# Kernel optimization log

Hardware: AMD Instinct MI355X
Metric: run time of the kernel (lower is better)

The kernel has to match this reference:

```python
import jax, jax.numpy as jnp
import numpy as np

N = 10000      # nodes
E = 160000     # edges
D_IN = 512
D_H = 512
P_DROP = 0.2


def _glorot(key, shape):
    lim = float(np.sqrt(6.0 / (shape[0] + shape[1])))
    return jax.random.uniform(key, shape, jnp.float32, -lim, lim)


def setup_inputs() -> dict:
    key = jax.random.key(0)
    ks = jax.random.split(key, 8)
    h = jax.random.normal(ks[0], (N, D_IN), jnp.float32)
    src = jax.random.randint(ks[1], (E,), 0, N)
    dst = jax.random.randint(ks[2], (E,), 0, N)
    edge_weight = jax.random.uniform(ks[3], (E,), jnp.float32)
    W0 = _glorot(ks[4], (D_IN, D_H))
    W1 = _glorot(ks[5], (D_H, D_H))
    W2 = _glorot(ks[6], (D_H, D_H))
    b0 = jnp.zeros((D_H,), jnp.float32)
    b1 = jnp.zeros((D_H,), jnp.float32)
    b2 = jnp.zeros((D_H,), jnp.float32)
    return dict(h=h, src=src, dst=dst, edge_weight=edge_weight,
                W0=W0, b0=b0, W1=W1, b1=b1, W2=W2, b2=b2)


def _dropout(x, key):
    keep = jax.random.bernoulli(key, 1.0 - P_DROP, x.shape)
    return jnp.where(keep, x / (1.0 - P_DROP), 0.0)


def _graph_conv(x, src, dst, ew, W, b, act):
    # DGL GraphConv, norm='both', weight=True, bias=True, with edge_weight.
    ones = jnp.ones((src.shape[0],), x.dtype)
    deg_out = jnp.maximum(jax.ops.segment_sum(ones, src, num_segments=N), 1.0)
    deg_in = jnp.maximum(jax.ops.segment_sum(ones, dst, num_segments=N), 1.0)
    x = x * (deg_out ** -0.5)[:, None]          # src norm
    msg = x[src] * ew[:, None]                  # [E, D] gather + edge weight
    agg = jax.ops.segment_sum(msg, dst, num_segments=N)  # scatter-add
    out = (agg @ W) * (deg_in ** -0.5)[:, None] + b
    return act(out) if act is not None else out


def reference(h, src, dst, edge_weight, W0, b0, W1, b1, W2, b2):
    dk = jax.random.split(jax.random.key(42), 3)
    x = _dropout(h, dk[0])
    x = _graph_conv(x, src, dst, edge_weight, W0, b0, jax.nn.elu)
    x = _dropout(x, dk[1])
    x = _graph_conv(x, src, dst, edge_weight, W1, b1, jax.nn.elu)
    x = _dropout(x, dk[2])
    x = _graph_conv(x, src, dst, edge_weight, W2, b2, None)
    return x
```

## Files before the change

kernel.cpp:

```cpp
#include <hip/hip_runtime.h>
#include <stdint.h>

#define N_NODES 10000
#define N_EDGES 160000
#define D 512
#define TOT (N_NODES * D)
#define M_PAD 10112
#define NMASK (TOT / 32)
#define AGG_BLKS 2500
#define MASK_BLKS 625

typedef _Float16 h8 __attribute__((ext_vector_type(8)));
typedef float f4 __attribute__((ext_vector_type(4)));

__host__ __device__ inline uint32_t rotl32(uint32_t v, int r) {
    return (v << r) | (v >> (32 - r));
}

__host__ __device__ inline void tf2x32(uint32_t k0, uint32_t k1,
                                       uint32_t& x0, uint32_t& x1) {
    uint32_t k2 = k0 ^ k1 ^ 0x1BD11BDAu;
    x0 += k0; x1 += k1;
    x0 += x1; x1 = rotl32(x1, 13); x1 ^= x0;
    x0 += x1; x1 = rotl32(x1, 15); x1 ^= x0;
    x0 += x1; x1 = rotl32(x1, 26); x1 ^= x0;
    x0 += x1; x1 = rotl32(x1,  6); x1 ^= x0;
    x0 += k1; x1 += k2 + 1u;
    x0 += x1; x1 = rotl32(x1, 17); x1 ^= x0;
    x0 += x1; x1 = rotl32(x1, 29); x1 ^= x0;
    x0 += x1; x1 = rotl32(x1, 16); x1 ^= x0;
    x0 += x1; x1 = rotl32(x1, 24); x1 ^= x0;
    x0 += k2; x1 += k0 + 2u;
    x0 += x1; x1 = rotl32(x1, 13); x1 ^= x0;
    x0 += x1; x1 = rotl32(x1, 15); x1 ^= x0;
    x0 += x1; x1 = rotl32(x1, 26); x1 ^= x0;
    x0 += x1; x1 = rotl32(x1,  6); x1 ^= x0;
    x0 += k0; x1 += k1 + 3u;
    x0 += x1; x1 = rotl32(x1, 17); x1 ^= x0;
    x0 += x1; x1 = rotl32(x1, 29); x1 ^= x0;
    x0 += x1; x1 = rotl32(x1, 16); x1 ^= x0;
    x0 += x1; x1 = rotl32(x1, 24); x1 ^= x0;
    x0 += k1; x1 += k2 + 4u;
    x0 += x1; x1 = rotl32(x1, 13); x1 ^= x0;
    x0 += x1; x1 = rotl32(x1, 15); x1 ^= x0;
    x0 += x1; x1 = rotl32(x1, 26); x1 ^= x0;
    x0 += x1; x1 = rotl32(x1,  6); x1 ^= x0;
    x0 += k2; x1 += k0 + 5u;
}

__device__ __forceinline__ uint32_t dropout_bit(uint32_t k0, uint32_t k1, uint32_t j) {
    uint32_t c0 = 0u, c1 = j;
    tf2x32(k0, k1, c0, c1);
    uint32_t bits = c0 ^ c1;
    float u = __uint_as_float((bits >> 9) | 0x3f800000u) - 1.0f;
    return (u < 0.8f) ? 1u : 0u;
}

#define HIST_BLKS 625
#define WCONV_BLKS 192
#define PRE_BLKS (HIST_BLKS + WCONV_BLKS + 5000)
__global__ __launch_bounds__(256)
void pre_kernel(const int* __restrict__ src, const int* __restrict__ dst,
                int* __restrict__ deg_out, int* __restrict__ deg_in,
                const float* __restrict__ W0, const float* __restrict__ W1,
                const float* __restrict__ W2, _Float16* __restrict__ Wt,
                const float* __restrict__ x, _Float16* __restrict__ y,
                uint32_t k0, uint32_t k1) {
    __shared__ float tile[64][65];
    int b = blockIdx.x;
    int t = threadIdx.x;
    if (b < HIST_BLKS) {
        int e = b * 256 + t;
        if (e < N_EDGES) {
            atomicAdd(&deg_out[src[e]], 1);
            atomicAdd(&deg_in[dst[e]], 1);
        }
    } else if (b < HIST_BLKS + WCONV_BLKS) {
        int b2 = b - HIST_BLKS;
        int bx = b2 & 7, by = (b2 >> 3) & 7, bz = b2 >> 6;
        const float* W = (bz == 0) ? W0 : (bz == 1) ? W1 : W2;
        _Float16* T = Wt + (size_t)bz * 512 * 512;
        int r0 = by * 64, c0 = bx * 64;
        int c = t & 63, rq = t >> 6;
#pragma unroll
        for (int i = 0; i < 16; ++i) {
            int r = rq + i * 4;
            tile[r][c] = W[(size_t)(r0 + r) * 512 + c0 + c];
        }
        __syncthreads();
        int k = t & 63, nq = t >> 6;
#pragma unroll
        for (int i = 0; i < 16; ++i) {
            int n = nq + i * 4;
            T[(size_t)(c0 + n) * 512 + r0 + k] = (_Float16)tile[k][n];
        }
    } else {
        int b3 = b - HIST_BLKS - WCONV_BLKS;
        int j = (b3 * 256 + t) * 4;
        if (j >= TOT) return;
        float4 xv = *(const float4*)&x[j];
        _Float16 r[4];
        uint32_t jj = (uint32_t)j;
#pragma unroll
        for (int i = 0; i < 4; ++i) {
            float g = dropout_bit(k0, k1, jj + (uint32_t)i) ? 1.0f : 0.0f;
            float xi = (&xv.x)[i];
            r[i] = (_Float16)(g * (xi * 1.25f));
        }
        *(ushort4*)&y[j] = *(ushort4*)r;
    }
}

__global__ __launch_bounds__(1024)
void scan_kernel(const int* __restrict__ deg_in, const int* __restrict__ deg_out,
                 int* __restrict__ row_ptr,
                 float* __restrict__ rn_in, float* __restrict__ rn_out) {
    __shared__ int wsum[16];
    int tid = threadIdx.x;
    int lane = tid & 63, wv = tid >> 6;
    int base = tid * 10;
    int v[10];
    int tot = 0;
#pragma unroll
    for (int i = 0; i < 10; ++i) {
        int idx = base + i;
        v[i] = (idx < N_NODES) ? deg_in[idx] : 0;
        tot += v[i];
    }
    int s = tot;
#pragma unroll
    for (int off = 1; off < 64; off <<= 1) {
        int t = __shfl_up(s, off, 64);
        if (lane >= off) s += t;
    }
    if (lane == 63) wsum[wv] = s;
    __syncthreads();
    if (wv == 0 && lane < 16) {
        int ws = wsum[lane];
#pragma unroll
        for (int off = 1; off < 16; off <<= 1) {
            int t = __shfl_up(ws, off, 64);
            if (lane >= off) ws += t;
        }
        wsum[lane] = ws;
    }
    __syncthreads();
    int run = ((wv > 0) ? wsum[wv - 1] : 0) + (s - tot);
#pragma unroll
    for (int i = 0; i < 10; ++i) {
        int idx = base + i;
        if (idx < N_NODES) {
            row_ptr[idx] = run;
            rn_in[idx]  = 1.0f / sqrtf(fmaxf((float)v[i], 1.0f));
            rn_out[idx] = 1.0f / sqrtf(fmaxf((float)deg_out[idx], 1.0f));
        }
        run += v[i];
    }
    if (tid == 1023) row_ptr[N_NODES] = wsum[15];
}

__global__ void fill_kernel(const int* __restrict__ src, const int* __restrict__ dst,
                            const float* __restrict__ ew, const int* __restrict__ row_ptr,
                            const float* __restrict__ rn_out,
                            int* __restrict__ cursor, int2* __restrict__ csr) {
    int e = blockIdx.x * 256 + threadIdx.x;
    if (e >= N_EDGES) return;
    int v = dst[e];
    int sn = src[e];
    int pos = atomicAdd(&cursor[v], 1);
    int idx = row_ptr[v] + pos;
    csr[idx] = make_int2(sn, __float_as_int(ew[e] * rn_out[sn]));
}

__global__ __launch_bounds__(256)
void aggregate_kernel(const _Float16* __restrict__ y, const int* __restrict__ row_ptr,
                      const int2* __restrict__ csr, _Float16* __restrict__ agg,
                      uint32_t* __restrict__ mask, uint32_t mk0, uint32_t mk1) {
    int b = blockIdx.x;
    if (b >= AGG_BLKS) {
        if (mask == nullptr) return;
        int gtid = (b - AGG_BLKS) * 256 + threadIdx.x;
        if (gtid < NMASK) {
            uint32_t w = 0, jb = (uint32_t)gtid * 32u;
#pragma unroll 4
            for (int i = 0; i < 32; ++i)
                w |= dropout_bit(mk0, mk1, jb + (uint32_t)i) << i;
            mask[gtid] = w;
        }
        return;
    }
    int node = b * 4 + (threadIdx.x >> 6);
    int lane = threadIdx.x & 63;
    int beg = row_ptr[node], end = row_ptr[node + 1];
    const _Float16* yl = y + lane * 8;
    float acc[8] = {0, 0, 0, 0, 0, 0, 0, 0};
    int k = beg;
    for (; k + 7 < end; k += 8) {
        int2 e[8];
#pragma unroll
        for (int i = 0; i < 8; ++i) e[i] = csr[k + i];
        h8 v[8];
#pragma unroll
        for (int i = 0; i < 8; ++i) v[i] = *(const h8*)&yl[(size_t)e[i].x * 512];
#pragma unroll
        for (int i = 0; i < 8; ++i) {
            float w = __int_as_float(e[i].y);
#pragma unroll
            for (int j = 0; j < 8; ++j) acc[j] += w * (float)v[i][j];
        }
    }
    for (; k < end; ++k) {
        int2 e0 = csr[k];
        float w = __int_as_float(e0.y);
        h8 v = *(const h8*)&yl[(size_t)e0.x * 512];
#pragma unroll
        for (int j = 0; j < 8; ++j) acc[j] += w * (float)v[j];
    }
    _Float16 r[8];
#pragma unroll
    for (int j = 0; j < 8; ++j) r[j] = (_Float16)acc[j];
    *(h8*)&agg[(size_t)node * 512 + lane * 8] = *(h8*)r;
}

#define GBK 128
#define LDA2 136
__global__ __launch_bounds__(256)
void gemm_kernel(const _Float16* __restrict__ A, const _Float16* __restrict__ Wt,
                 const float* __restrict__ bias, const float* __restrict__ rn_in,
                 _Float16* __restrict__ yout, float* __restrict__ fout,
                 int mode, const uint32_t* __restrict__ mask) {
    __shared__ _Float16 As[64 * LDA2];
    __shared__ _Float16 Bs[64 * LDA2];
    int tid = threadIdx.x;
    int wv = tid >> 6, lane = tid & 63;

    int f = blockIdx.x;
    int T = (f & 7) * 158 + (f >> 3);
    int row0 = (T >> 3) * 64, col0 = (T & 7) * 64;

    int wr = wv >> 1, wc = wv & 1;

    f4 acc[2][2];
#pragma unroll
    for (int i = 0; i < 2; ++i)
#pragma unroll
        for (int j = 0; j < 2; ++j) acc[i][j] = (f4){0.f, 0.f, 0.f, 0.f};

    int r = tid >> 2;
    int cseg = (tid & 3) * 32;
    const _Float16* gA = A  + (size_t)(row0 + r) * 512 + cseg;
    const _Float16* gB = Wt + (size_t)(col0 + r) * 512 + cseg;
    _Float16* wA = &As[r * LDA2 + cseg];
    _Float16* wB = &Bs[r * LDA2 + cseg];

    const _Float16* fa = &As[(wr * 32 + (lane & 15)) * LDA2 + (lane >> 4) * 8];
    const _Float16* fb = &Bs[(wc * 32 + (lane & 15)) * LDA2 + (lane >> 4) * 8];

    h8 ra[4], rb[4];
#pragma unroll
    for (int i = 0; i < 4; ++i) {
        ra[i] = *(const h8*)(gA + i * 8);
        rb[i] = *(const h8*)(gB + i * 8);
    }

    for (int kk = 0; kk < 512; kk += GBK) {
#pragma unroll
        for (int i = 0; i < 4; ++i) {
            *(h8*)(wA + i * 8) = ra[i];
            *(h8*)(wB + i * 8) = rb[i];
        }
        __syncthreads();
        if (kk + GBK < 512) {
#pragma unroll
            for (int i = 0; i < 4; ++i) {
                ra[i] = *(const h8*)(gA + kk + GBK + i * 8);
                rb[i] = *(const h8*)(gB + kk + GBK + i * 8);
            }
        }
#pragma unroll
        for (int s = 0; s < 4; ++s) {
            h8 af0 = *(const h8*)(fa + s * 32);
            h8 af1 = *(const h8*)(fa + 16 * LDA2 + s * 32);
            h8 bf0 = *(const h8*)(fb + s * 32);
            h8 bf1 = *(const h8*)(fb + 16 * LDA2 + s * 32);
            acc[0][0] = __builtin_amdgcn_mfma_f32_16x16x32_f16(af0, bf0, acc[0][0], 0, 0, 0);
            acc[0][1] = __builtin_amdgcn_mfma_f32_16x16x32_f16(af0, bf1, acc[0][1], 0, 0, 0);
            acc[1][0] = __builtin_amdgcn_mfma_f32_16x16x32_f16(af1, bf0, acc[1][0], 0, 0, 0);
            acc[1][1] = __builtin_amdgcn_mfma_f32_16x16x32_f16(af1, bf1, acc[1][1], 0, 0, 0);
        }
        __syncthreads();
    }

    int mbase = row0 + wr * 32;
    int nbase = col0 + wc * 32;
#pragma unroll
    for (int mt = 0; mt < 2; ++mt) {
#pragma unroll
        for (int nt = 0; nt < 2; ++nt) {
            int gr0 = mbase + mt * 16 + (lane >> 4) * 4;
            int gc = nbase + nt * 16 + (lane & 15);
            float bcol = bias[gc];
#pragma unroll
            for (int i = 0; i < 4; ++i) {
                int gr = gr0 + i;
                if (gr >= N_NODES) continue;
                float v = acc[mt][nt][i] * rn_in[gr] + bcol;
                if (mode == 0) {
                    v = (v > 0.f) ? v : (__expf(v) - 1.0f);
                    uint32_t j = (uint32_t)(gr * 512 + gc);
                    uint32_t g = (mask[j >> 5] >> (j & 31)) & 1u;
                    v = g ? (v * 1.25f) : 0.0f;
                    yout[(size_t)gr * 512 + gc] = (_Float16)v;
                } else {
                    fout[(size_t)gr * 512 + gc] = v;
                }
            }
        }
    }
}

extern "C" void kernel_launch(void* const* d_in, const int* in_sizes, int n_in,
                              void* d_out, int out_size, void* d_ws, size_t ws_size,
                              hipStream_t stream) {
    const float* h   = (const float*)d_in[0];
    const int*   src = (const int*)d_in[1];
    const int*   dst = (const int*)d_in[2];
    const float* ew  = (const float*)d_in[3];
    const float* W0  = (const float*)d_in[4];
    const float* b0  = (const float*)d_in[5];
    const float* W1  = (const float*)d_in[6];
    const float* b1  = (const float*)d_in[7];
    const float* W2  = (const float*)d_in[8];
    const float* b2  = (const float*)d_in[9];
    const float* bl[3] = {b0, b1, b2};
    float* out = (float*)d_out;

    char* ws = (char*)d_ws;
    _Float16* y16  = (_Float16*)ws; ws += (size_t)TOT * 2;
    _Float16* aggF = (_Float16*)ws; ws += (size_t)M_PAD * 512 * 2;
    _Float16* Wt   = (_Float16*)ws; ws += (size_t)3 * 512 * 512 * 2;
    int* degi_in  = (int*)ws;  ws += N_NODES * 4;
    int* degi_out = (int*)ws;  ws += N_NODES * 4;
    int* cursor   = (int*)ws;  ws += N_NODES * 4;
    int* row_ptr  = (int*)ws;  ws += (N_NODES + 1) * 4;
    ws = (char*)(((uintptr_t)ws + 15) & ~(uintptr_t)15);
    int2* csr     = (int2*)ws; ws += (size_t)N_EDGES * 8;
    float* rn_in  = (float*)ws; ws += N_NODES * 4;
    float* rn_out = (float*)ws; ws += N_NODES * 4;
    uint32_t* maskbuf = (uint32_t*)ws; ws += (size_t)NMASK * 4;

    hipMemsetAsync(degi_in, 0, 3 * N_NODES * 4, stream);

    uint32_t dk[3][2];
    for (int i = 0; i < 3; ++i) {
        uint32_t c0 = 0u, c1 = (uint32_t)i;
        tf2x32(0u, 42u, c0, c1);
        dk[i][0] = c0; dk[i][1] = c1;
    }

    pre_kernel<<<PRE_BLKS, 256, 0, stream>>>(src, dst, degi_out, degi_in,
                                             W0, W1, W2, Wt, h, y16,
                                             dk[0][0], dk[0][1]);
    scan_kernel<<<1, 1024, 0, stream>>>(degi_in, degi_out, row_ptr, rn_in, rn_out);
    fill_kernel<<<(N_EDGES + 255) / 256, 256, 0, stream>>>(src, dst, ew, row_ptr,
                                                           rn_out, cursor, csr);

    for (int l = 0; l < 3; ++l) {
        uint32_t* mk = (l < 2) ? maskbuf : nullptr;
        uint32_t mk0 = (l < 2) ? dk[l + 1][0] : 0u;
        uint32_t mk1 = (l < 2) ? dk[l + 1][1] : 0u;
        aggregate_kernel<<<AGG_BLKS + MASK_BLKS, 256, 0, stream>>>(
            y16, row_ptr, csr, aggF, mk, mk0, mk1);
        int mode = (l < 2) ? 0 : 1;
        gemm_kernel<<<1264, 256, 0, stream>>>(
            aggF, Wt + (size_t)l * 512 * 512, bl[l], rn_in,
            y16, out, mode, maskbuf);
    }
}
```

Before: 316.3 us.

## Fuse neighbor aggregation and GEMM per 16-node tile with ping-pong buffers

Replaces the separate aggregate and GEMM kernels with one fused kernel per layer. Each 64-thread block gathers 16 nodes' neighbor features into LDS, then multiplies them by the full 512x512 weight using MFMA, applying the bias/ELU/dropout epilogue in place. Both dropout masks are now generated up front in the pre-kernel into separate buffers, and activations ping-pong between two buffers. This removes the intermediate aggregate round trip through memory and two launches per layer. In exchange, only 625 single-wave blocks run, giving low occupancy to hide gather latency, and every block re-reads the whole weight matrix from cache.

```diff
diff --git a/kernel.cpp b/kernel.cpp
--- a/kernel.cpp
+++ b/kernel.cpp
@@ -5,10 +5,7 @@
 #define N_EDGES 160000
 #define D 512
 #define TOT (N_NODES * D)
-#define M_PAD 10112
 #define NMASK (TOT / 32)
-#define AGG_BLKS 2500
-#define MASK_BLKS 625
 
 typedef _Float16 h8 __attribute__((ext_vector_type(8)));
 typedef float f4 __attribute__((ext_vector_type(4)));
@@ -58,14 +55,18 @@
 
 #define HIST_BLKS 625
 #define WCONV_BLKS 192
-#define PRE_BLKS (HIST_BLKS + WCONV_BLKS + 5000)
+#define DROP_BLKS 5000
+#define MASKG_BLKS 625
+#define PRE_BLKS (HIST_BLKS + WCONV_BLKS + DROP_BLKS + 2 * MASKG_BLKS)
 __global__ __launch_bounds__(256)
 void pre_kernel(const int* __restrict__ src, const int* __restrict__ dst,
                 int* __restrict__ deg_out, int* __restrict__ deg_in,
                 const float* __restrict__ W0, const float* __restrict__ W1,
                 const float* __restrict__ W2, _Float16* __restrict__ Wt,
                 const float* __restrict__ x, _Float16* __restrict__ y,
-                uint32_t k0, uint32_t k1) {
+                uint32_t k0, uint32_t k1,
+                uint32_t m1k0, uint32_t m1k1, uint32_t* __restrict__ mask1,
+                uint32_t m2k0, uint32_t m2k1, uint32_t* __restrict__ mask2) {
     __shared__ float tile[64][65];
     int b = blockIdx.x;
     int t = threadIdx.x;
@@ -94,7 +95,7 @@
             int n = nq + i * 4;
             T[(size_t)(c0 + n) * 512 + r0 + k] = (_Float16)tile[k][n];
         }
-    } else {
+    } else if (b < HIST_BLKS + WCONV_BLKS + DROP_BLKS) {
         int b3 = b - HIST_BLKS - WCONV_BLKS;
         int j = (b3 * 256 + t) * 4;
         if (j >= TOT) return;
@@ -108,6 +109,18 @@
             r[i] = (_Float16)(g * (xi * 1.25f));
         }
         *(ushort4*)&y[j] = *(ushort4*)r;
+    } else {
+        int b4 = b - HIST_BLKS - WCONV_BLKS - DROP_BLKS;
+        int which = b4 / MASKG_BLKS;
+        int gtid = (b4 % MASKG_BLKS) * 256 + t;
+        uint32_t mk0 = which ? m2k0 : m1k0;
+        uint32_t mk1 = which ? m2k1 : m1k1;
+        uint32_t* m = which ? mask2 : mask1;
+        uint32_t w = 0, jb = (uint32_t)gtid * 32u;
+#pragma unroll 4
+        for (int i = 0; i < 32; ++i)
+            w |= dropout_bit(mk0, mk1, jb + (uint32_t)i) << i;
+        m[gtid] = w;
     }
 }
 
@@ -172,150 +185,125 @@
     csr[idx] = make_int2(sn, __float_as_int(ew[e] * rn_out[sn]));
 }
 
-__global__ __launch_bounds__(256)
-void aggregate_kernel(const _Float16* __restrict__ y, const int* __restrict__ row_ptr,
-                      const int2* __restrict__ csr, _Float16* __restrict__ agg,
-                      uint32_t* __restrict__ mask, uint32_t mk0, uint32_t mk1) {
-    int b = blockIdx.x;
-    if (b >= AGG_BLKS) {
-        if (mask == nullptr) return;
-        int gtid = (b - AGG_BLKS) * 256 + threadIdx.x;
-        if (gtid < NMASK) {
-            uint32_t w = 0, jb = (uint32_t)gtid * 32u;
-#pragma unroll 4
-            for (int i = 0; i < 32; ++i)
-                w |= dropout_bit(mk0, mk1, jb + (uint32_t)i) << i;
-            mask[gtid] = w;
-        }
-        return;
-    }
-    int node = b * 4 + (threadIdx.x >> 6);
-    int lane = threadIdx.x & 63;
-    int beg = row_ptr[node], end = row_ptr[node + 1];
-    const _Float16* yl = y + lane * 8;
-    float acc[8] = {0, 0, 0, 0, 0, 0, 0, 0};
-    int k = beg;
-    for (; k + 7 < end; k += 8) {
-        int2 e[8];
-#pragma unroll
-        for (int i = 0; i < 8; ++i) e[i] = csr[k + i];
-        h8 v[8];
-#pragma unroll
-        for (int i = 0; i < 8; ++i) v[i] = *(const h8*)&yl[(size_t)e[i].x * 512];
-#pragma unroll
-        for (int i = 0; i < 8; ++i) {
-            float w = __int_as_float(e[i].y);
-#pragma unroll
-            for (int j = 0; j < 8; ++j) acc[j] += w * (float)v[i][j];
-        }
-    }
-    for (; k < end; ++k) {
-        int2 e0 = csr[k];
-        float w = __int_as_float(e0.y);
-        h8 v = *(const h8*)&yl[(size_t)e0.x * 512];
-#pragma unroll
-        for (int j = 0; j < 8; ++j) acc[j] += w * (float)v[j];
-    }
-    _Float16 r[8];
-#pragma unroll
-    for (int j = 0; j < 8; ++j) r[j] = (_Float16)acc[j];
-    *(h8*)&agg[(size_t)node * 512 + lane * 8] = *(h8*)r;
-}
-
-#define GBK 128
-#define LDA2 136
-__global__ __launch_bounds__(256)
-void gemm_kernel(const _Float16* __restrict__ A, const _Float16* __restrict__ Wt,
-                 const float* __restrict__ bias, const float* __restrict__ rn_in,
-                 _Float16* __restrict__ yout, float* __restrict__ fout,
-                 int mode, const uint32_t* __restrict__ mask) {
-    __shared__ _Float16 As[64 * LDA2];
-    __shared__ _Float16 Bs[64 * LDA2];
-    int tid = threadIdx.x;
-    int wv = tid >> 6, lane = tid & 63;
-
-    int f = blockIdx.x;
-    int T = (f & 7) * 158 + (f >> 3);
-    int row0 = (T >> 3) * 64, col0 = (T & 7) * 64;
-
-    int wr = wv >> 1, wc = wv & 1;
-
-    f4 acc[2][2];
-#pragma unroll
-    for (int i = 0; i < 2; ++i)
-#pragma unroll
-        for (int j = 0; j < 2; ++j) acc[i][j] = (f4){0.f, 0.f, 0.f, 0.f};
-
-    int r = tid >> 2;
-    int cseg = (tid & 3) * 32;
-    const _Float16* gA = A  + (size_t)(row0 + r) * 512 + cseg;
-    const _Float16* gB = Wt + (size_t)(col0 + r) * 512 + cseg;
-    _Float16* wA = &As[r * LDA2 + cseg];
-    _Float16* wB = &Bs[r * LDA2 + cseg];
-
-    const _Float16* fa = &As[(wr * 32 + (lane & 15)) * LDA2 + (lane >> 4) * 8];
-    const _Float16* fb = &Bs[(wc * 32 + (lane & 15)) * LDA2 + (lane >> 4) * 8];
-
-    h8 ra[4], rb[4];
-#pragma unroll
-    for (int i = 0; i < 4; ++i) {
-        ra[i] = *(const h8*)(gA + i * 8);
-        rb[i] = *(const h8*)(gB + i * 8);
-    }
-
-    for (int kk = 0; kk < 512; kk += GBK) {
+#define LDF 520
+__global__ __launch_bounds__(64)
+void fused_kernel(const _Float16* __restrict__ yin, const int* __restrict__ row_ptr,
+                  const int2* __restrict__ csr, const _Float16* __restrict__ Wt,
+                  const float* __restrict__ bias, const float* __restrict__ rn_in,
+                  const uint32_t* __restrict__ mask,
+                  _Float16* __restrict__ yout, float* __restrict__ fout, int mode) {
+    __shared__ _Float16 AT[16 * LDF];
+    const int lane = threadIdx.x;
+    const int base = blockIdx.x * 16;
+    const _Float16* yl = yin + lane * 8;
+
+    for (int i = 0; i < 16; ++i) {
+        int beg = row_ptr[base + i], end = row_ptr[base + i + 1];
+        float acc[8] = {0, 0, 0, 0, 0, 0, 0, 0};
+        int k = beg;
+        for (; k + 15 < end; k += 16) {
+            int2 e[16];
+#pragma unroll
+            for (int u = 0; u < 16; ++u) e[u] = csr[k + u];
+            h8 v[16];
+#pragma unroll
+            for (int u = 0; u < 16; ++u) v[u] = *(const h8*)&yl[(size_t)e[u].x * 512];
+#pragma unroll
+            for (int u = 0; u < 16; ++u) {
+                float w = __int_as_float(e[u].y);
+#pragma unroll
+                for (int j = 0; j < 8; ++j) acc[j] += w * (float)v[u][j];
+            }
+        }
+        for (; k + 3 < end; k += 4) {
+            int2 e[4];
+#pragma unroll
+            for (int u = 0; u < 4; ++u) e[u] = csr[k + u];
+            h8 v[4];
+#pragma unroll
+            for (int u = 0; u < 4; ++u) v[u] = *(const h8*)&yl[(size_t)e[u].x * 512];
+#pragma unroll
+            for (int u = 0; u < 4; ++u) {
+                float w = __int_as_float(e[u].y);
+#pragma unroll
+                for (int j = 0; j < 8; ++j) acc[j] += w * (float)v[u][j];
+            }
+        }
+        for (; k < end; ++k) {
+            int2 e0 = csr[k];
+            float w = __int_as_float(e0.y);
+            h8 v = *(const h8*)&yl[(size_t)e0.x * 512];
+#pragma unroll
+            for (int j = 0; j < 8; ++j) acc[j] += w * (float)v[j];
+        }
+        _Float16 r[8];
+#pragma unroll
+        for (int j = 0; j < 8; ++j) r[j] = (_Float16)acc[j];
+        *(h8*)&AT[i * LDF + lane * 8] = *(h8*)r;
+    }
+    __syncthreads();
+
+    h8 a[16];
+#pragma unroll
+    for (int ks = 0; ks < 16; ++ks)
+        a[ks] = *(const h8*)&AT[(lane & 15) * LDF + ks * 32 + (lane >> 4) * 8];
+    __syncthreads();
+
+    const int r0 = (lane >> 4) * 4;
+    float rn[4];
+#pragma unroll
+    for (int i = 0; i < 4; ++i) rn[i] = rn_in[base + r0 + i];
+
+    const _Float16* bp = Wt + (size_t)(lane & 15) * 512 + (lane >> 4) * 8;
+
+    h8 bfA[16], bfB[16];
+    auto bload = [&](h8* d, int nt) {
+        const _Float16* bn = bp + (size_t)nt * (16 * 512);
+#pragma unroll
+        for (int ks = 0; ks < 16; ++ks) d[ks] = *(const h8*)(bn + ks * 32);
+    };
+    auto mmaepi = [&](const h8* bf, int nt) {
+        f4 c0 = (f4){0.f, 0.f, 0.f, 0.f}, c1 = c0, c2 = c0, c3 = c0;
+#pragma unroll
+        for (int q = 0; q < 4; ++q) {
+            c0 = __builtin_amdgcn_mfma_f32_16x16x32_f16(a[q],      bf[q],      c0, 0, 0, 0);
+            c1 = __builtin_amdgcn_mfma_f32_16x16x32_f16(a[4 + q],  bf[4 + q],  c1, 0, 0, 0);
+            c2 = __builtin_amdgcn_mfma_f32_16x16x32_f16(a[8 + q],  bf[8 + q],  c2, 0, 0, 0);
+            c3 = __builtin_amdgcn_mfma_f32_16x16x32_f16(a[12 + q], bf[12 + q], c3, 0, 0, 0);
+        }
+        f4 c = (c0 + c1) + (c2 + c3);
+        int col = nt * 16 + (lane & 15);
+        float bcol = bias[col];
 #pragma unroll
         for (int i = 0; i < 4; ++i) {
-            *(h8*)(wA + i * 8) = ra[i];
-            *(h8*)(wB + i * 8) = rb[i];
-        }
+            int gr = base + r0 + i;
+            float v = c[i] * rn[i] + bcol;
+            if (mode == 0) {
+                v = (v > 0.f) ? v : (__expf(v) - 1.0f);
+                uint32_t j = (uint32_t)(gr * 512 + col);
+                uint32_t g = (mask[j >> 5] >> (j & 31)) & 1u;
+                v = g ? (v * 1.25f) : 0.0f;
+                AT[(r0 + i) * LDF + col] = (_Float16)v;
+            } else {
+                fout[(size_t)gr * 512 + col] = v;
+            }
+        }
+    };
+
+    bload(bfA, 0);
+    for (int nt = 0; nt < 32; nt += 2) {
+        bload(bfB, nt + 1);
+        mmaepi(bfA, nt);
+        if (nt + 2 < 32) bload(bfA, nt + 2);
+        mmaepi(bfB, nt + 1);
+    }
+
+    if (mode == 0) {
         __syncthreads();
-        if (kk + GBK < 512) {
-#pragma unroll
-            for (int i = 0; i < 4; ++i) {
-                ra[i] = *(const h8*)(gA + kk + GBK + i * 8);
-                rb[i] = *(const h8*)(gB + kk + GBK + i * 8);
-            }
-        }
-#pragma unroll
-        for (int s = 0; s < 4; ++s) {
-            h8 af0 = *(const h8*)(fa + s * 32);
-            h8 af1 = *(const h8*)(fa + 16 * LDA2 + s * 32);
-            h8 bf0 = *(const h8*)(fb + s * 32);
-            h8 bf1 = *(const h8*)(fb + 16 * LDA2 + s * 32);
-            acc[0][0] = __builtin_amdgcn_mfma_f32_16x16x32_f16(af0, bf0, acc[0][0], 0, 0, 0);
-            acc[0][1] = __builtin_amdgcn_mfma_f32_16x16x32_f16(af0, bf1, acc[0][1], 0, 0, 0);
-            acc[1][0] = __builtin_amdgcn_mfma_f32_16x16x32_f16(af1, bf0, acc[1][0], 0, 0, 0);
-            acc[1][1] = __builtin_amdgcn_mfma_f32_16x16x32_f16(af1, bf1, acc[1][1], 0, 0, 0);
-        }
-        __syncthreads();
-    }
-
-    int mbase = row0 + wr * 32;
-    int nbase = col0 + wc * 32;
-#pragma unroll
-    for (int mt = 0; mt < 2; ++mt) {
-#pragma unroll
-        for (int nt = 0; nt < 2; ++nt) {
-            int gr0 = mbase + mt * 16 + (lane >> 4) * 4;
-            int gc = nbase + nt * 16 + (lane & 15);
-            float bcol = bias[gc];
-#pragma unroll
-            for (int i = 0; i < 4; ++i) {
-                int gr = gr0 + i;
-                if (gr >= N_NODES) continue;
-                float v = acc[mt][nt][i] * rn_in[gr] + bcol;
-                if (mode == 0) {
-                    v = (v > 0.f) ? v : (__expf(v) - 1.0f);
-                    uint32_t j = (uint32_t)(gr * 512 + gc);
-                    uint32_t g = (mask[j >> 5] >> (j & 31)) & 1u;
-                    v = g ? (v * 1.25f) : 0.0f;
-                    yout[(size_t)gr * 512 + gc] = (_Float16)v;
-                } else {
-                    fout[(size_t)gr * 512 + gc] = v;
-                }
-            }
-        }
+#pragma unroll
+        for (int rr = 0; rr < 16; ++rr)
+            *(h8*)&yout[(size_t)(base + rr) * 512 + lane * 8] =
+                *(const h8*)&AT[rr * LDF + lane * 8];
     }
 }
 
@@ -332,12 +320,11 @@
     const float* b1  = (const float*)d_in[7];
     const float* W2  = (const float*)d_in[8];
     const float* b2  = (const float*)d_in[9];
-    const float* bl[3] = {b0, b1, b2};
     float* out = (float*)d_out;
 
     char* ws = (char*)d_ws;
     _Float16* y16  = (_Float16*)ws; ws += (size_t)TOT * 2;
-    _Float16* aggF = (_Float16*)ws; ws += (size_t)M_PAD * 512 * 2;
+    _Float16* y16b = (_Float16*)ws; ws += (size_t)TOT * 2;
     _Float16* Wt   = (_Float16*)ws; ws += (size_t)3 * 512 * 512 * 2;
     int* degi_in  = (int*)ws;  ws += N_NODES * 4;
     int* degi_out = (int*)ws;  ws += N_NODES * 4;
@@ -347,7 +334,8 @@
     int2* csr     = (int2*)ws; ws += (size_t)N_EDGES * 8;
     float* rn_in  = (float*)ws; ws += N_NODES * 4;
     float* rn_out = (float*)ws; ws += N_NODES * 4;
-    uint32_t* maskbuf = (uint32_t*)ws; ws += (size_t)NMASK * 4;
+    uint32_t* mask1 = (uint32_t*)ws; ws += (size_t)NMASK * 4;
+    uint32_t* mask2 = (uint32_t*)ws; ws += (size_t)NMASK * 4;
 
     hipMemsetAsync(degi_in, 0, 3 * N_NODES * 4, stream);
 
@@ -360,20 +348,17 @@
 
     pre_kernel<<<PRE_BLKS, 256, 0, stream>>>(src, dst, degi_out, degi_in,
                                              W0, W1, W2, Wt, h, y16,
-                                             dk[0][0], dk[0][1]);
+                                             dk[0][0], dk[0][1],
+                                             dk[1][0], dk[1][1], mask1,
+                                             dk[2][0], dk[2][1], mask2);
     scan_kernel<<<1, 1024, 0, stream>>>(degi_in, degi_out, row_ptr, rn_in, rn_out);
     fill_kernel<<<(N_EDGES + 255) / 256, 256, 0, stream>>>(src, dst, ew, row_ptr,
                                                            rn_out, cursor, csr);
 
-    for (int l = 0; l < 3; ++l) {
-        uint32_t* mk = (l < 2) ? maskbuf : nullptr;
-        uint32_t mk0 = (l < 2) ? dk[l + 1][0] : 0u;
-        uint32_t mk1 = (l < 2) ? dk[l + 1][1] : 0u;
-        aggregate_kernel<<<AGG_BLKS + MASK_BLKS, 256, 0, stream>>>(
-            y16, row_ptr, csr, aggF, mk, mk0, mk1);
-        int mode = (l < 2) ? 0 : 1;
-        gemm_kernel<<<1264, 256, 0, stream>>>(
-            aggF, Wt + (size_t)l * 512 * 512, bl[l], rn_in,
-            y16, out, mode, maskbuf);
-    }
-}
+    fused_kernel<<<625, 64, 0, stream>>>(y16, row_ptr, csr, Wt,
+                                         b0, rn_in, mask1, y16b, nullptr, 0);
+    fused_kernel<<<625, 64, 0, stream>>>(y16b, row_ptr, csr, Wt + (size_t)512 * 512,
+                                         b1, rn_in, mask2, y16, nullptr, 0);
+    fused_kernel<<<625, 64, 0, stream>>>(y16, row_ptr, csr, Wt + (size_t)2 * 512 * 512,
+                                         b2, rn_in, nullptr, nullptr, out, 1);
+}
```

Measured after the change: 449.4 us. 1.42x slower.
